# Performance work log

Measured on AMD Instinct MI355X. Metric: run time of the kernel, lower is better.

## Reference

```python
import jax, jax.numpy as jnp
import numpy as np

B, L, D, H, K = 4, 2048, 256, 8, 32
DH = D // H
DE = 64          # d_edge
CLIP = 32        # relpos_clip


def _ln(x, g, b):
    mu = x.mean(-1, keepdims=True)
    var = ((x - mu) ** 2).mean(-1, keepdims=True)
    return (x - mu) / jnp.sqrt(var + 1e-5) * g + b


def _gelu(x):
    return jax.nn.gelu(x, approximate=False)  # torch nn.GELU default = exact erf


def _masked_softmax(logits, mask):
    logits = jnp.where(mask == 0, jnp.finfo(logits.dtype).min, logits)
    return jax.nn.softmax(logits, axis=-1)


def setup_inputs() -> dict:
    key = jax.random.key(0)
    ks = jax.random.split(key, 24)
    s = 0.02
    w = lambda i, shape: jax.random.normal(ks[i], shape, jnp.float32) * s
    p = {}
    p['x'] = jax.random.normal(ks[0], (B, L, D), jnp.float32)
    p['mask'] = jax.random.randint(ks[1], (B, L), 0, 2, jnp.int32)
    p['nbr_idx'] = jax.random.randint(ks[2], (B, L, K), 0, L, jnp.int32)
    p['nbr_mask'] = jax.random.randint(ks[3], (B, L, K), 0, 2, jnp.int32)
    p['rel_pos'] = jax.random.randint(ks[4], (B, L, K), 0, 2 * CLIP + 1, jnp.int32)
    p['g1'] = jnp.ones((D,)); p['b1'] = jnp.zeros((D,))
    p['wq'] = w(5, (D, D)); p['wk'] = w(6, (D, D)); p['wv'] = w(7, (D, D))
    p['relpos_emb'] = w(8, (2 * CLIP + 1, DE))
    p['we1'] = w(9, (DE, D)); p['be1'] = jnp.zeros((D,))
    p['we2'] = w(10, (D, 1)); p['be2'] = jnp.zeros((1,))
    p['wg1'] = w(11, (2 * D, D)); p['bg1'] = jnp.zeros((D,))
    p['wg2'] = w(12, (D, D)); p['bg2'] = jnp.zeros((D,))
    p['wlo'] = w(13, (D, D)); p['blo'] = jnp.zeros((D,))
    p['wqkv'] = w(14, (D, 3 * D)); p['wgo'] = w(15, (D, D))
    p['wf1'] = w(16, (D, D)); p['bf1'] = jnp.zeros((D,))
    p['wf2'] = w(17, (D, 2)); p['bf2'] = jnp.zeros((2,))
    p['g2'] = jnp.ones((D,)); p['b2'] = jnp.zeros((D,))
    p['wff1'] = w(18, (D, 4 * D)); p['bff1'] = jnp.zeros((4 * D,))
    p['wff2'] = w(19, (4 * D, D)); p['bff2'] = jnp.zeros((D,))
    return p


def _block(x, mask, nbr_idx, nbr_mask, rel_pos,
           g1, b1, wq, wk, wv, relpos_emb, we1, be1, we2, be2,
           wg1, bg1, wg2, bg2, wlo, blo, wqkv, wgo,
           wf1, bf1, wf2, bf2, g2, b2, wff1, bff1, wff2, bff2):
    mf = mask.astype(x.dtype)                       # [B,L]
    h = _ln(x, g1, b1)

    # ---- local graph attention (gather over K neighbors) ----
    neigh = jax.vmap(lambda hb, ib: hb[ib])(h, nbr_idx)     # [B,L,K,D]
    q = (h @ wq)[:, :, None, :]                             # [B,L,1,D]
    k = neigh @ wk                                          # [B,L,K,D]
    v = neigh @ wv
    attn = (q * k).sum(-1) / np.sqrt(D).astype(np.float32)  # [B,L,K]
    rel = jnp.clip(rel_pos, -CLIP, CLIP) + CLIP
    e = relpos_emb[rel]                                     # [B,L,K,DE]
    attn = attn + (_gelu(e @ we1 + be1) @ we2 + be2)[..., 0]
    amask = nbr_mask * mask[:, :, None]
    w = _masked_softmax(attn, amask)
    agg = jnp.einsum('blk,blkd->bld', w, v)
    agg = agg @ wlo + blo
    g = jax.nn.sigmoid(_gelu(jnp.concatenate([h, agg], -1) @ wg1 + bg1) @ wg2 + bg2)
    h_local = (h + g * agg) * mf[..., None]

    # ---- global linear attention ----
    qkv = h @ wqkv
    qg, kg, vg = jnp.split(qkv, 3, axis=-1)
    to_heads = lambda z: z.reshape(B, L, H, DH).transpose(0, 2, 1, 3)  # [B,H,L,DH]
    qg, kg, vg = to_heads(qg), to_heads(kg), to_heads(vg)
    phi = lambda z: jax.nn.elu(z) + 1.0
    qg, kg = phi(qg), phi(kg)
    m = mf[:, None, :, None]
    kg = kg * m
    vg = vg * m
    kv = jnp.einsum('bhld,bhlm->bhdm', kg, vg)
    z = 1.0 / (jnp.einsum('bhld,bhd->bhl', qg, kg.sum(axis=2)) + 1e-6)
    y = jnp.einsum('bhld,bhdm->bhlm', qg, kv) * z[..., None]
    y = y.transpose(0, 2, 1, 3).reshape(B, L, D)
    y = (y @ wgo) * mf[..., None]
    h_global = h + y

    # ---- gated fusion (softmax over 2 branches) ----
    fw = jax.nn.softmax(_gelu(h @ wf1 + bf1) @ wf2 + bf2, axis=-1)
    yc = fw[..., 0:1] * h_local + fw[..., 1:2] * h_global
    x2 = x + (yc - x)  # DropPath is identity in eval mode

    # ---- FFN ----
    hn = _ln(x2, g2, b2)
    ffn = _gelu(hn @ wff1 + bff1) @ wff2 + bff2
    out = (x2 + ffn) * mf[..., None]
    return out


def reference(x, mask, nbr_idx, nbr_mask, rel_pos,
              g1, b1, wq, wk, wv, relpos_emb, we1, be1, we2, be2,
              wg1, bg1, wg2, bg2, wlo, blo, wqkv, wgo,
              wf1, bf1, wf2, bf2, g2, b2, wff1, bff1, wff2, bff2):
    return _block(x, mask, nbr_idx, nbr_mask, rel_pos,
                  g1, b1, wq, wk, wv, relpos_emb, we1, be1, we2, be2,
                  wg1, bg1, wg2, bg2, wlo, blo, wqkv, wgo,
                  wf1, bf1, wf2, bf2, g2, b2, wff1, bff1, wff2, bff2)
```

## Files before the change

kernel.cpp:

```cpp
#include <hip/hip_runtime.h>
#include <math.h>

#define LSEQ 2048
#define BB 4
#define DD 256
#define NROWS (BB*LSEQ)
#define LDBIG 1792

typedef unsigned short u16;
typedef unsigned int u32;
typedef short s16x8 __attribute__((ext_vector_type(8)));
typedef float f32x4 __attribute__((ext_vector_type(4)));

__device__ __forceinline__ float gelu_f(float x){
    return 0.5f*x*(1.0f+erff(x*0.70710678118654752440f));
}
__device__ __forceinline__ float phi_f(float z){ return z>0.f ? z+1.f : expf(z); }
__device__ __forceinline__ float bf2f(u16 u){ union{u32 i; float f;} x; x.i = ((u32)u)<<16; return x.f; }
__device__ __forceinline__ u16 f2bf(float f){ union{float f; u32 i;} x; x.f = f; u32 r = (x.i + 0x7fff + ((x.i>>16)&1)) >> 16; return (u16)r; }

struct TransDesc { const float* src; int dstoff; int K; int N; int tstart; };
struct TransArgs { TransDesc d[11]; };

__global__ __launch_bounds__(256) void prep_kernel(
    TransArgs args, u16* __restrict__ WT,
    const float* __restrict__ x, const float* __restrict__ g1,
    const float* __restrict__ b1, u16* __restrict__ h,
    const float* __restrict__ emb, const float* __restrict__ we1,
    const float* __restrict__ be1, const float* __restrict__ we2,
    const float* __restrict__ be2, float* __restrict__ btab,
    float* __restrict__ kvz)
{
    int bid = blockIdx.x;
    if (bid < 1280){
        int z = 0;
        #pragma unroll
        for (int i=1;i<11;++i) if (bid >= args.d[i].tstart) z = i;
        TransDesc e = args.d[z];
        int tid = bid - e.tstart;
        int ntx = e.N >> 5;
        int kt = tid / ntx, nt = tid - kt*ntx;
        __shared__ float tile[32][33];
        int tx = threadIdx.x & 31, ty = threadIdx.x >> 5;
        #pragma unroll
        for (int i=0;i<4;++i){
            int k = kt*32 + ty + i*8;
            tile[ty+i*8][tx] = e.src[(size_t)k*e.N + nt*32 + tx];
        }
        __syncthreads();
        #pragma unroll
        for (int i=0;i<4;++i){
            int n = nt*32 + ty + i*8;
            WT[e.dstoff + (size_t)n*e.K + kt*32 + tx] = f2bf(tile[tx][ty+i*8]);
        }
    } else if (bid < 9472){
        int r = bid - 1280; int t = threadIdx.x;
        size_t i = (size_t)r*DD + t;
        float v = x[i];
        float s = v, ss = v*v;
        #pragma unroll
        for (int o=32;o>=1;o>>=1){ s += __shfl_xor(s,o); ss += __shfl_xor(ss,o); }
        __shared__ float sh[8];
        int wave = t>>6, lane = t&63;
        if (lane==0){ sh[wave]=s; sh[4+wave]=ss; }
        __syncthreads();
        float S  = sh[0]+sh[1]+sh[2]+sh[3];
        float SS = sh[4]+sh[5]+sh[6]+sh[7];
        float mu  = S*(1.f/DD);
        float var = SS*(1.f/DD) - mu*mu;
        float inv = rsqrtf(var + 1e-5f);
        h[i] = f2bf((v-mu)*inv*g1[t] + b1[t]);
    } else if (bid < 9537){
        int r = bid - 9472; int j = threadIdx.x;
        float acc = be1[j];
        #pragma unroll 8
        for (int d=0; d<64; ++d) acc += emb[r*64+d]*we1[d*256+j];
        float tv = gelu_f(acc)*we2[j];
        #pragma unroll
        for (int o=32;o>=1;o>>=1) tv += __shfl_xor(tv,o);
        __shared__ float sh2[4];
        int wave = j>>6, lane = j&63;
        if (lane==0) sh2[wave]=tv;
        __syncthreads();
        if (j==0) btab[r] = sh2[0]+sh2[1]+sh2[2]+sh2[3] + be2[0];
    } else {
        int idx = (bid - 9537)*256 + threadIdx.x;
        kvz[idx] = 0.f;
    }
}

template<int ACT, bool FINAL, typename CT>
__device__ __forceinline__ void mgemm_core(
    const u16* __restrict__ A0, const u16* __restrict__ A1, int kswitch, int lda,
    const u16* __restrict__ WT, int Kd,
    const float* __restrict__ bias, int actcol,
    CT* __restrict__ C, int ldc,
    const u16* __restrict__ addsrc, const int* __restrict__ rowmask,
    int row0, int col0)
{
    __shared__ u16 ldsA[4096];
    __shared__ u16 ldsB[8192];
    int t = threadIdx.x;
    int l = t & 63, w = t >> 6;
    int wm = w >> 1, wn = w & 1;

    int s_ar = t >> 2, s_ao = t & 3;
    int aidx1 = (s_ar>>4)*1024 + s_ao*128 + (s_ar&15)*8;
    int aidx2 = aidx1 + 4*128;
    int s_bc = t >> 1, s_bo = (t & 1)*4;
    int bbase = (s_bc>>4)*1024 + (s_bc&15)*8;

    f32x4 acc[2][4];
    #pragma unroll
    for (int mf=0;mf<2;++mf)
        #pragma unroll
        for (int nf=0;nf<4;++nf)
            acc[mf][nf] = (f32x4){0.f,0.f,0.f,0.f};

    uint4 av1, av2, bv0, bv1, bv2, bv3;
    {
        const u16* ap = A0 + (size_t)(row0+s_ar)*lda;
        av1 = *(const uint4*)(ap + s_ao*8);
        av2 = *(const uint4*)(ap + 32 + s_ao*8);
        const u16* bp = WT + (size_t)(col0 + s_bc)*Kd + s_bo*8;
        bv0 = *(const uint4*)(bp); bv1 = *(const uint4*)(bp+8);
        bv2 = *(const uint4*)(bp+16); bv3 = *(const uint4*)(bp+24);
    }

    for (int k0 = 0; k0 < Kd; k0 += 64){
        __syncthreads();
        *(uint4*)&ldsA[aidx1] = av1;
        *(uint4*)&ldsA[aidx2] = av2;
        *(uint4*)&ldsB[bbase + (s_bo  )*128] = bv0;
        *(uint4*)&ldsB[bbase + (s_bo+1)*128] = bv1;
        *(uint4*)&ldsB[bbase + (s_bo+2)*128] = bv2;
        *(uint4*)&ldsB[bbase + (s_bo+3)*128] = bv3;
        __syncthreads();
        int kn = k0 + 64;
        if (kn < Kd){
            const u16* Ab = A0; int kk = kn;
            if (kn >= kswitch){ Ab = A1; kk = kn - kswitch; }
            const u16* ap = Ab + (size_t)(row0+s_ar)*lda + kk;
            av1 = *(const uint4*)(ap + s_ao*8);
            av2 = *(const uint4*)(ap + 32 + s_ao*8);
            const u16* bp = WT + (size_t)(col0 + s_bc)*Kd + kn + s_bo*8;
            bv0 = *(const uint4*)(bp); bv1 = *(const uint4*)(bp+8);
            bv2 = *(const uint4*)(bp+16); bv3 = *(const uint4*)(bp+24);
        }
        #pragma unroll
        for (int s=0;s<2;++s){
            s16x8 af[2], bfr[4];
            #pragma unroll
            for (int mf=0;mf<2;++mf) af[mf] = *(s16x8*)&ldsA[(wm*2+mf)*1024 + (s*4+(l>>4))*128 + (l&15)*8];
            #pragma unroll
            for (int nf=0;nf<4;++nf) bfr[nf] = *(s16x8*)&ldsB[(wn*4+nf)*1024 + (s*4+(l>>4))*128 + (l&15)*8];
            #pragma unroll
            for (int mf=0; mf<2; ++mf)
                #pragma unroll
                for (int nf=0; nf<4; ++nf)
                    acc[mf][nf] = __builtin_amdgcn_mfma_f32_16x16x32_bf16(af[mf], bfr[nf], acc[mf][nf], 0,0,0);
        }
    }

    int lrow = (l>>4)*4, lcol = l&15;
    #pragma unroll
    for (int mf=0; mf<2; ++mf){
        #pragma unroll
        for (int nf=0; nf<4; ++nf){
            int col = col0 + wn*64 + nf*16 + lcol;
            float bv;
            if (ACT==1) bv = (col >= actcol) ? bias[col-actcol] : 0.f;
            else        bv = bias ? bias[col] : 0.f;
            #pragma unroll
            for (int i=0;i<4;++i){
                int row = row0 + wm*32 + mf*16 + lrow + i;
                float v = acc[mf][nf][i] + bv;
                if (ACT==1){ if (col >= actcol) v = gelu_f(v); }
                else if (ACT==2) v = 1.f/(1.f+expf(-v));
                if (FINAL){
                    float mfv = (float)rowmask[row];
                    v = (bf2f(addsrc[(size_t)row*ldc + col]) + v) * mfv;
                }
                if constexpr (sizeof(CT)==2) C[(size_t)row*ldc+col] = (CT)f2bf(v);
                else                         C[(size_t)row*ldc+col] = v;
            }
        }
    }
}

template<int ACT, bool FINAL, typename CT>
__global__ __launch_bounds__(256) void mgemm(
    const u16* __restrict__ A0, const u16* __restrict__ A1, int kswitch, int lda,
    const u16* __restrict__ WT, int Kd,
    const float* __restrict__ bias, int actcol,
    CT* __restrict__ C, int ldc,
    const u16* __restrict__ addsrc, const int* __restrict__ rowmask)
{
    mgemm_core<ACT,FINAL,CT>(A0,A1,kswitch,lda,WT,Kd,bias,actcol,C,ldc,addsrc,rowmask,
                             blockIdx.x*64, blockIdx.y*128);
}

struct DualCfg { const u16* A; const u16* WT; const float* bias; u16* C; };
__global__ __launch_bounds__(256) void mgemm_dual(DualCfg c0, DualCfg c1)
{
    DualCfg c = blockIdx.z ? c1 : c0;
    mgemm_core<0,false,u16>(c.A, c.A, 1<<30, 256, c.WT, 256, c.bias, 0, c.C, 256,
                            nullptr, nullptr, blockIdx.x*64, blockIdx.y*128);
}

__global__ __launch_bounds__(256) void nattn_kernel(
    const u16* __restrict__ nb,
    const int* __restrict__ nbr_idx, const int* __restrict__ nbr_mask,
    const int* __restrict__ rel_pos, const int* __restrict__ mask,
    const float* __restrict__ btab, u16* __restrict__ agg)
{
    int r = blockIdx.x;
    int b = r >> 11;
    int t = threadIdx.x, lane = t&63, wave = t>>6;
    __shared__ float s_w[32];
    __shared__ float s_agg[4][256];
    uint2 qu = *(const uint2*)&nb[(size_t)r*LDBIG + lane*4];
    float q0 = bf2f(qu.x&0xffff), q1 = bf2f(qu.x>>16);
    float q2 = bf2f(qu.y&0xffff), q3 = bf2f(qu.y>>16);
    int mrow = mask[r];

    uint2 kreg[8], vreg[8];
    #pragma unroll
    for (int j=0;j<8;++j){
        int idx = nbr_idx[r*32 + wave*8 + j];
        size_t grow = ((size_t)(b<<11) + idx)*LDBIG;
        kreg[j] = *(const uint2*)&nb[grow + 256 + lane*4];
        vreg[j] = *(const uint2*)&nb[grow + 512 + lane*4];
    }
    float d[8];
    #pragma unroll
    for (int j=0;j<8;++j){
        d[j] = q0*bf2f(kreg[j].x&0xffff) + q1*bf2f(kreg[j].x>>16)
             + q2*bf2f(kreg[j].y&0xffff) + q3*bf2f(kreg[j].y>>16);
    }
    #define CMB(a,b,s) ({ float _t = (lane&(s)) ? (a) : (b); float _r = __shfl_xor(_t,(s)); (lane&(s)) ? ((b)+_r) : ((a)+_r); })
    float e10 = CMB(d[0],d[1],1), e11 = CMB(d[2],d[3],1);
    float e12 = CMB(d[4],d[5],1), e13 = CMB(d[6],d[7],1);
    float e20 = CMB(e10,e11,2),   e21 = CMB(e12,e13,2);
    float e3  = CMB(e20,e21,4);
    #undef CMB
    e3 += __shfl_xor(e3,8); e3 += __shfl_xor(e3,16); e3 += __shfl_xor(e3,32);
    if (lane < 8){
        int k = wave*8 + lane;
        int rp = rel_pos[r*32+k];
        rp = rp < -32 ? -32 : (rp > 32 ? 32 : rp);
        float logit = e3*0.0625f + btab[rp+32];
        int am = nbr_mask[r*32+k] * mrow;
        s_w[k] = am ? logit : -3.402823466e38f;
    }
    __syncthreads();
    if (wave==0){
        float lg = (lane<32) ? s_w[lane] : -3.402823466e38f;
        float m = lg;
        #pragma unroll
        for (int o=16;o>=1;o>>=1) m = fmaxf(m, __shfl_xor(m,o));
        float e = (lane<32) ? expf(lg-m) : 0.f;
        float ssum = e;
        #pragma unroll
        for (int o=16;o>=1;o>>=1) ssum += __shfl_xor(ssum,o);
        if (lane<32) s_w[lane] = e/ssum;
    }
    __syncthreads();
    float4 av = {0.f,0.f,0.f,0.f};
    #pragma unroll
    for (int j=0;j<8;++j){
        float wk = s_w[wave*8 + j];
        av.x += wk*bf2f(vreg[j].x&0xffff); av.y += wk*bf2f(vreg[j].x>>16);
        av.z += wk*bf2f(vreg[j].y&0xffff); av.w += wk*bf2f(vreg[j].y>>16);
    }
    *(float4*)&s_agg[wave][lane*4] = av;
    __syncthreads();
    float sum = s_agg[0][t]+s_agg[1][t]+s_agg[2][t]+s_agg[3][t];
    agg[(size_t)r*256 + t] = f2bf(sum);
}

__global__ __launch_bounds__(256) void linstats_kernel(
    const u16* __restrict__ qkv, const int* __restrict__ mask,
    float* __restrict__ kv, float* __restrict__ ksum)
{
    int blk = blockIdx.x;
    int bh = blk >> 4, ch = blk & 15;
    int b = bh >> 3, hh = bh & 7;
    int t = threadIdx.x;
    int d = t >> 3, m4 = (t & 7)*4;
    __shared__ float sk[8][32], sv[8][32];
    float a0=0,a1=0,a2=0,a3=0, aks=0;
    int l0 = ch*128;
    int half = t >> 7, tt = t & 127;
    int lr = tt >> 4, e2 = (tt & 15)*2;
    for (int g8=0; g8<16; ++g8){
        int l = l0 + g8*8 + lr;
        size_t base = ((size_t)b*LSEQ + l)*LDBIG + (half ? 1280 : 1024) + hh*32 + e2;
        u32 u = *(const u32*)&qkv[base];
        float mf = (float)mask[b*LSEQ + l];
        float x0 = bf2f((u16)(u & 0xffff));
        float x1 = bf2f((u16)(u >> 16));
        if (half==0){ sk[lr][e2] = phi_f(x0)*mf; sk[lr][e2+1] = phi_f(x1)*mf; }
        else        { sv[lr][e2] = x0*mf;        sv[lr][e2+1] = x1*mf; }
        __syncthreads();
        #pragma unroll
        for (int rr=0;rr<8;++rr){
            float kd = sk[rr][d];
            a0 += kd*sv[rr][m4]; a1 += kd*sv[rr][m4+1];
            a2 += kd*sv[rr][m4+2]; a3 += kd*sv[rr][m4+3];
            if ((t&7)==0) aks += kd;
        }
        __syncthreads();
    }
    size_t kb = (size_t)bh*1024 + d*32 + m4;
    atomicAdd(&kv[kb+0],a0); atomicAdd(&kv[kb+1],a1);
    atomicAdd(&kv[kb+2],a2); atomicAdd(&kv[kb+3],a3);
    if ((t&7)==0) atomicAdd(&ksum[bh*32+d], aks);
}

__global__ __launch_bounds__(256) void linapply_kernel(
    const u16* __restrict__ qkv, const float* __restrict__ kv,
    const float* __restrict__ ksum, u16* __restrict__ y)
{
    int r = blockIdx.x; int b = r >> 11;
    int t = threadIdx.x;
    __shared__ float sq[256];
    if (t < 128){
        u32 u = *(const u32*)&qkv[(size_t)r*LDBIG + 768 + t*2];
        sq[t*2]   = phi_f(bf2f((u16)(u & 0xffff)));
        sq[t*2+1] = phi_f(bf2f((u16)(u >> 16)));
    }
    __syncthreads();
    int hh = t>>5, m = t&31;
    const float* kvb = &kv[(size_t)((b<<3)+hh)*1024 + m];
    const float* ksb = &ksum[((b<<3)+hh)*32];
    const float* sqh = &sq[hh*32];
    float acc=0.f, az=0.f;
    #pragma unroll
    for (int dd=0; dd<32; ++dd){
        float qd = sqh[dd];
        acc += qd * kvb[dd*32];
        az  += qd * ksb[dd];
    }
    y[(size_t)r*256 + t] = f2bf(acc / (az + 1e-6f));
}

__global__ __launch_bounds__(128) void combine_kernel(
    const u16* __restrict__ h, const u16* __restrict__ agglo,
    const u16* __restrict__ g, const u16* __restrict__ ygo,
    const u16* __restrict__ bigout, const float* __restrict__ wf2,
    const float* __restrict__ bf2v, const int* __restrict__ mask,
    const float* __restrict__ g2, const float* __restrict__ b2,
    u16* __restrict__ x2, u16* __restrict__ hn)
{
    int r = blockIdx.x, t = threadIdx.x;
    int wave = t>>6, lane = t&63;
    u32 fu = *(const u32*)&bigout[(size_t)r*LDBIG + 1536 + t*2];
    float fa = bf2f((u16)(fu&0xffff)), fb = bf2f((u16)(fu>>16));
    int dd = t*2;
    float p0 = fa*wf2[dd*2]   + fb*wf2[dd*2+2];
    float p1 = fa*wf2[dd*2+1] + fb*wf2[dd*2+3];
    #pragma unroll
    for (int o=32;o>=1;o>>=1){ p0 += __shfl_xor(p0,o); p1 += __shfl_xor(p1,o); }
    __shared__ float shp[4];
    if (lane==0){ shp[wave]=p0; shp[2+wave]=p1; }
    __syncthreads();
    float P0 = shp[0]+shp[1]+bf2v[0], P1 = shp[2]+shp[3]+bf2v[1];
    float mx = fmaxf(P0,P1);
    float e0 = expf(P0-mx), e1 = expf(P1-mx);
    float f0 = e0/(e0+e1), f1v = e1/(e0+e1);
    size_t i = (size_t)r*DD + t*2;
    float mf = (float)mask[r];
    u32 hu = *(const u32*)&h[i],  au = *(const u32*)&agglo[i];
    u32 gu = *(const u32*)&g[i],  yu = *(const u32*)&ygo[i];
    float hv0 = bf2f((u16)(hu&0xffff)), hv1 = bf2f((u16)(hu>>16));
    float ag0 = bf2f((u16)(au&0xffff)), ag1 = bf2f((u16)(au>>16));
    float gg0 = bf2f((u16)(gu&0xffff)), gg1 = bf2f((u16)(gu>>16));
    float yy0 = bf2f((u16)(yu&0xffff)), yy1 = bf2f((u16)(yu>>16));
    float v0 = f0*((hv0 + gg0*ag0)*mf) + f1v*(hv0 + yy0*mf);
    float v1 = f0*((hv1 + gg1*ag1)*mf) + f1v*(hv1 + yy1*mf);
    *(u32*)&x2[i] = (u32)f2bf(v0) | ((u32)f2bf(v1)<<16);
    float s = v0+v1, ss = v0*v0+v1*v1;
    #pragma unroll
    for (int o=32;o>=1;o>>=1){ s += __shfl_xor(s,o); ss += __shfl_xor(ss,o); }
    __shared__ float sh[4];
    if (lane==0){ sh[wave]=s; sh[2+wave]=ss; }
    __syncthreads();
    float S  = sh[0]+sh[1];
    float SS = sh[2]+sh[3];
    float mu  = S*(1.f/DD);
    float var = SS*(1.f/DD) - mu*mu;
    float inv = rsqrtf(var + 1e-5f);
    int j0 = t*2;
    float o0 = (v0-mu)*inv*g2[j0]   + b2[j0];
    float o1 = (v1-mu)*inv*g2[j0+1] + b2[j0+1];
    *(u32*)&hn[i] = (u32)f2bf(o0) | ((u32)f2bf(o1)<<16);
}

extern "C" void kernel_launch(void* const* d_in, const int* in_sizes, int n_in,
                              void* d_out, int out_size, void* d_ws, size_t ws_size,
                              hipStream_t stream)
{
    const float* x        = (const float*)d_in[0];
    const int*   mask     = (const int*)  d_in[1];
    const int*   nbr_idx  = (const int*)  d_in[2];
    const int*   nbr_mask = (const int*)  d_in[3];
    const int*   rel_pos  = (const int*)  d_in[4];
    const float* g1   = (const float*)d_in[5];
    const float* b1   = (const float*)d_in[6];
    const float* wq   = (const float*)d_in[7];
    const float* wk   = (const float*)d_in[8];
    const float* wv   = (const float*)d_in[9];
    const float* relpos_emb = (const float*)d_in[10];
    const float* we1  = (const float*)d_in[11];
    const float* be1  = (const float*)d_in[12];
    const float* we2  = (const float*)d_in[13];
    const float* be2  = (const float*)d_in[14];
    const float* wg1  = (const float*)d_in[15];
    const float* bg1  = (const float*)d_in[16];
    const float* wg2  = (const float*)d_in[17];
    const float* bg2  = (const float*)d_in[18];
    const float* wlo  = (const float*)d_in[19];
    const float* blo  = (const float*)d_in[20];
    const float* wqkv = (const float*)d_in[21];
    const float* wgo  = (const float*)d_in[22];
    const float* wf1  = (const float*)d_in[23];
    const float* bf1  = (const float*)d_in[24];
    const float* wf2  = (const float*)d_in[25];
    const float* bf2  = (const float*)d_in[26];
    const float* g2   = (const float*)d_in[27];
    const float* b2   = (const float*)d_in[28];
    const float* wff1 = (const float*)d_in[29];
    const float* bff1 = (const float*)d_in[30];
    const float* wff2 = (const float*)d_in[31];
    const float* bff2 = (const float*)d_in[32];
    float* out = (float*)d_out;

    unsigned char* wsb = (unsigned char*)d_ws;
    u16* bigout  = (u16*)(wsb + ((size_t)0<<20));
    u16* h_bf    = (u16*)(wsb + ((size_t)30<<20));
    u16* agg_bf  = (u16*)(wsb + ((size_t)34<<20));
    u16* agglo_bf= (u16*)(wsb + ((size_t)38<<20));
    u16* x2y_bf  = (u16*)(wsb + ((size_t)42<<20));
    u16* tg_bf   = (u16*)(wsb + ((size_t)46<<20));
    u16* ygo_bf  = (u16*)(wsb + ((size_t)50<<20));
    u16* hn_bf   = (u16*)(wsb + ((size_t)54<<20));
    u16* WT      = (u16*)(wsb + ((size_t)58<<20));
    float* btab  = (float*)(wsb + ((size_t)61<<20));
    float* kvb   = btab + 128;
    float* ksb   = kvb + 32768;

    const int WT_BIG  = 0;
    const int WT_LO   = 458752;
    const int WT_G1   = 524288;
    const int WT_G2   = 655360;
    const int WT_GO   = 720896;
    const int WT_FF1  = 786432;
    const int WT_FF2  = 1048576;

    TransArgs ta;
    ta.d[0]  = { wq,   WT_BIG + 0,        256,  256,    0 };
    ta.d[1]  = { wk,   WT_BIG + 65536,    256,  256,   64 };
    ta.d[2]  = { wv,   WT_BIG + 131072,   256,  256,  128 };
    ta.d[3]  = { wqkv, WT_BIG + 196608,   256,  768,  192 };
    ta.d[4]  = { wf1,  WT_BIG + 393216,   256,  256,  384 };
    ta.d[5]  = { wlo,  WT_LO,             256,  256,  448 };
    ta.d[6]  = { wg1,  WT_G1,             512,  256,  512 };
    ta.d[7]  = { wg2,  WT_G2,             256,  256,  640 };
    ta.d[8]  = { wgo,  WT_GO,             256,  256,  704 };
    ta.d[9]  = { wff1, WT_FF1,            256, 1024,  768 };
    ta.d[10] = { wff2, WT_FF2,           1024,  256, 1024 };

    const int KBIG = 1<<30;
    dim3 blk(256);

    prep_kernel<<<9669, blk, 0, stream>>>(ta, WT, x, g1, b1, h_bf,
                                          relpos_emb, we1, be1, we2, be2, btab, kvb);
    mgemm<1,false,u16><<<dim3(128,14), blk, 0, stream>>>(h_bf, h_bf, KBIG, 256, WT+WT_BIG, 256, bf1, 1536, bigout, LDBIG, nullptr, nullptr);
    linstats_kernel<<<512, blk, 0, stream>>>(bigout, mask, kvb, ksb);
    linapply_kernel<<<NROWS, blk, 0, stream>>>(bigout, kvb, ksb, x2y_bf);
    nattn_kernel<<<NROWS, blk, 0, stream>>>(bigout, nbr_idx, nbr_mask, rel_pos, mask, btab, agg_bf);
    {
        DualCfg cgo = { x2y_bf, WT+WT_GO, nullptr, ygo_bf };
        DualCfg clo = { agg_bf, WT+WT_LO, blo,     agglo_bf };
        mgemm_dual<<<dim3(128,2,2), blk, 0, stream>>>(cgo, clo);
    }
    mgemm<1,false,u16><<<dim3(128,2), blk, 0, stream>>>(h_bf, agglo_bf, 256, 256, WT+WT_G1, 512, bg1, 0, tg_bf, 256, nullptr, nullptr);
    mgemm<2,false,u16><<<dim3(128,2), blk, 0, stream>>>(tg_bf, tg_bf, KBIG, 256, WT+WT_G2, 256, bg2, 0, agg_bf, 256, nullptr, nullptr);
    combine_kernel<<<NROWS, dim3(128), 0, stream>>>(h_bf, agglo_bf, agg_bf, ygo_bf, bigout, wf2, bf2, mask, g2, b2, x2y_bf, hn_bf);
    mgemm<1,false,u16><<<dim3(128,8), blk, 0, stream>>>(hn_bf, hn_bf, KBIG, 256, WT+WT_FF1, 256, bff1, 0, bigout, 1024, nullptr, nullptr);
    mgemm<0,true,float><<<dim3(128,2), blk, 0, stream>>>(bigout, bigout, KBIG, 1024, WT+WT_FF2, 1024, bff2, 0, out, 256, x2y_bf, mask);
}
```

Measured before the change: 277.6 us.

## Fold wlo into wg1, fuse linear-attn apply into neighbor attention, merge three GEMMs

```diff
diff --git a/kernel.cpp b/kernel.cpp
--- a/kernel.cpp
+++ b/kernel.cpp
@@ -12,6 +12,14 @@
 typedef short s16x8 __attribute__((ext_vector_type(8)));
 typedef float f32x4 __attribute__((ext_vector_type(4)));
 
+#define WT_BIG  0
+#define WT_LO   458752
+#define WT_G1   524288
+#define WT_G2   655360
+#define WT_GO   720896
+#define WT_FF1  786432
+#define WT_FF2  1048576
+
 __device__ __forceinline__ float gelu_f(float x){
     return 0.5f*x*(1.0f+erff(x*0.70710678118654752440f));
 }
@@ -19,7 +27,7 @@
 __device__ __forceinline__ float bf2f(u16 u){ union{u32 i; float f;} x; x.i = ((u32)u)<<16; return x.f; }
 __device__ __forceinline__ u16 f2bf(float f){ union{float f; u32 i;} x; x.f = f; u32 r = (x.i + 0x7fff + ((x.i>>16)&1)) >> 16; return (u16)r; }
 
-struct TransDesc { const float* src; int dstoff; int K; int N; int tstart; };
+struct TransDesc { const float* src; int dstoff; int srcK; int N; int dstStride; int tstart; };
 struct TransArgs { TransDesc d[11]; };
 
 __global__ __launch_bounds__(256) void prep_kernel(
@@ -29,10 +37,13 @@
     const float* __restrict__ emb, const float* __restrict__ we1,
     const float* __restrict__ be1, const float* __restrict__ we2,
     const float* __restrict__ be2, float* __restrict__ btab,
-    float* __restrict__ kvz)
+    float* __restrict__ kvz,
+    const float* __restrict__ wlo, const float* __restrict__ wg1,
+    const float* __restrict__ blo, const float* __restrict__ bg1,
+    float* __restrict__ bprime)
 {
     int bid = blockIdx.x;
-    if (bid < 1280){
+    if (bid < 1216){
         int z = 0;
         #pragma unroll
         for (int i=1;i<11;++i) if (bid >= args.d[i].tstart) z = i;
@@ -51,10 +62,10 @@
         #pragma unroll
         for (int i=0;i<4;++i){
             int n = nt*32 + ty + i*8;
-            WT[e.dstoff + (size_t)n*e.K + kt*32 + tx] = f2bf(tile[tx][ty+i*8]);
+            WT[e.dstoff + (size_t)n*e.dstStride + kt*32 + tx] = f2bf(tile[tx][ty+i*8]);
         }
-    } else if (bid < 9472){
-        int r = bid - 1280; int t = threadIdx.x;
+    } else if (bid < 9408){
+        int r = bid - 1216; int t = threadIdx.x;
         size_t i = (size_t)r*DD + t;
         float v = x[i];
         float s = v, ss = v*v;
@@ -70,8 +81,8 @@
         float var = SS*(1.f/DD) - mu*mu;
         float inv = rsqrtf(var + 1e-5f);
         h[i] = f2bf((v-mu)*inv*g1[t] + b1[t]);
-    } else if (bid < 9537){
-        int r = bid - 9472; int j = threadIdx.x;
+    } else if (bid < 9473){
+        int r = bid - 9408; int j = threadIdx.x;
         float acc = be1[j];
         #pragma unroll 8
         for (int d=0; d<64; ++d) acc += emb[r*64+d]*we1[d*256+j];
@@ -83,9 +94,24 @@
         if (lane==0) sh2[wave]=tv;
         __syncthreads();
         if (j==0) btab[r] = sh2[0]+sh2[1]+sh2[2]+sh2[3] + be2[0];
+    } else if (bid < 9605){
+        int idx = (bid - 9473)*256 + threadIdx.x;
+        kvz[idx] = 0.f;
+    } else if (bid < 9861){
+        int n = bid - 9605; int t = threadIdx.x;
+        __shared__ float shc[256];
+        shc[t] = wg1[(size_t)(256+t)*256 + n];
+        __syncthreads();
+        const float* wr = wlo + (size_t)t*256;
+        float a = 0.f;
+        #pragma unroll 8
+        for (int m=0;m<256;++m) a += wr[m]*shc[m];
+        WT[WT_G1 + (size_t)n*512 + 256 + t] = f2bf(a);
     } else {
-        int idx = (bid - 9537)*256 + threadIdx.x;
-        kvz[idx] = 0.f;
+        int t = threadIdx.x;
+        float a = bg1[t];
+        for (int m=0;m<256;++m) a += blo[m]*wg1[(size_t)(256+m)*256 + t];
+        bprime[t] = a;
     }
 }
 
@@ -200,25 +226,35 @@
                              blockIdx.x*64, blockIdx.y*128);
 }
 
-struct DualCfg { const u16* A; const u16* WT; const float* bias; u16* C; };
-__global__ __launch_bounds__(256) void mgemm_dual(DualCfg c0, DualCfg c1)
-{
-    DualCfg c = blockIdx.z ? c1 : c0;
-    mgemm_core<0,false,u16>(c.A, c.A, 1<<30, 256, c.WT, 256, c.bias, 0, c.C, 256,
-                            nullptr, nullptr, blockIdx.x*64, blockIdx.y*128);
-}
-
-__global__ __launch_bounds__(256) void nattn_kernel(
+struct GemmCfg { const u16* A0; const u16* A1; int kswitch; const u16* WT; int Kd;
+                 const float* bias; int act; u16* C; };
+__global__ __launch_bounds__(256) void mgemm_tri(GemmCfg c0, GemmCfg c1, GemmCfg c2)
+{
+    GemmCfg c = (blockIdx.z==0) ? c0 : ((blockIdx.z==1) ? c1 : c2);
+    if (c.act==1)
+        mgemm_core<1,false,u16>(c.A0, c.A1, c.kswitch, 256, c.WT, c.Kd, c.bias, 0,
+                                c.C, 256, nullptr, nullptr, blockIdx.x*64, blockIdx.y*128);
+    else
+        mgemm_core<0,false,u16>(c.A0, c.A1, c.kswitch, 256, c.WT, c.Kd, c.bias, 0,
+                                c.C, 256, nullptr, nullptr, blockIdx.x*64, blockIdx.y*128);
+}
+
+__global__ __launch_bounds__(256) void lg_kernel(
     const u16* __restrict__ nb,
     const int* __restrict__ nbr_idx, const int* __restrict__ nbr_mask,
     const int* __restrict__ rel_pos, const int* __restrict__ mask,
-    const float* __restrict__ btab, u16* __restrict__ agg)
-{
-    int r = blockIdx.x;
+    const float* __restrict__ btab, u16* __restrict__ agg,
+    const float* __restrict__ kv, const float* __restrict__ ksum,
+    u16* __restrict__ y)
+{
+    int bid = blockIdx.x;
+    int xcd = bid & 7, pos = bid >> 3;
+    int r = (xcd>>1)*2048 + (xcd&1)*1024 + pos;
     int b = r >> 11;
     int t = threadIdx.x, lane = t&63, wave = t>>6;
     __shared__ float s_w[32];
     __shared__ float s_agg[4][256];
+    __shared__ float sq[256];
     uint2 qu = *(const uint2*)&nb[(size_t)r*LDBIG + lane*4];
     float q0 = bf2f(qu.x&0xffff), q1 = bf2f(qu.x>>16);
     float q2 = bf2f(qu.y&0xffff), q3 = bf2f(qu.y>>16);
@@ -253,6 +289,11 @@
         int am = nbr_mask[r*32+k] * mrow;
         s_w[k] = am ? logit : -3.402823466e38f;
     }
+    if (t < 128){
+        u32 u = *(const u32*)&nb[(size_t)r*LDBIG + 768 + t*2];
+        sq[t*2]   = phi_f(bf2f((u16)(u & 0xffff)));
+        sq[t*2+1] = phi_f(bf2f((u16)(u >> 16)));
+    }
     __syncthreads();
     if (wave==0){
         float lg = (lane<32) ? s_w[lane] : -3.402823466e38f;
@@ -277,6 +318,19 @@
     __syncthreads();
     float sum = s_agg[0][t]+s_agg[1][t]+s_agg[2][t]+s_agg[3][t];
     agg[(size_t)r*256 + t] = f2bf(sum);
+
+    int hh = t>>5, m = t&31;
+    const float* kvb = &kv[(size_t)((b<<3)+hh)*1024 + m];
+    const float* ksb = &ksum[((b<<3)+hh)*32];
+    const float* sqh = &sq[hh*32];
+    float acc=0.f, az=0.f;
+    #pragma unroll
+    for (int dd=0; dd<32; ++dd){
+        float qd = sqh[dd];
+        acc += qd * kvb[dd*32];
+        az  += qd * ksb[dd];
+    }
+    y[(size_t)r*256 + t] = f2bf(acc / (az + 1e-6f));
 }
 
 __global__ __launch_bounds__(256) void linstats_kernel(
@@ -284,16 +338,16 @@
     float* __restrict__ kv, float* __restrict__ ksum)
 {
     int blk = blockIdx.x;
-    int bh = blk >> 4, ch = blk & 15;
+    int bh = blk >> 6, ch = blk & 63;
     int b = bh >> 3, hh = bh & 7;
     int t = threadIdx.x;
     int d = t >> 3, m4 = (t & 7)*4;
     __shared__ float sk[8][32], sv[8][32];
     float a0=0,a1=0,a2=0,a3=0, aks=0;
-    int l0 = ch*128;
+    int l0 = ch*32;
     int half = t >> 7, tt = t & 127;
     int lr = tt >> 4, e2 = (tt & 15)*2;
-    for (int g8=0; g8<16; ++g8){
+    for (int g8=0; g8<4; ++g8){
         int l = l0 + g8*8 + lr;
         size_t base = ((size_t)b*LSEQ + l)*LDBIG + (half ? 1280 : 1024) + hh*32 + e2;
         u32 u = *(const u32*)&qkv[base];
@@ -316,33 +370,6 @@
     atomicAdd(&kv[kb+0],a0); atomicAdd(&kv[kb+1],a1);
     atomicAdd(&kv[kb+2],a2); atomicAdd(&kv[kb+3],a3);
     if ((t&7)==0) atomicAdd(&ksum[bh*32+d], aks);
-}
-
-__global__ __launch_bounds__(256) void linapply_kernel(
-    const u16* __restrict__ qkv, const float* __restrict__ kv,
-    const float* __restrict__ ksum, u16* __restrict__ y)
-{
-    int r = blockIdx.x; int b = r >> 11;
-    int t = threadIdx.x;
-    __shared__ float sq[256];
-    if (t < 128){
-        u32 u = *(const u32*)&qkv[(size_t)r*LDBIG + 768 + t*2];
-        sq[t*2]   = phi_f(bf2f((u16)(u & 0xffff)));
-        sq[t*2+1] = phi_f(bf2f((u16)(u >> 16)));
-    }
-    __syncthreads();
-    int hh = t>>5, m = t&31;
-    const float* kvb = &kv[(size_t)((b<<3)+hh)*1024 + m];
-    const float* ksb = &ksum[((b<<3)+hh)*32];
-    const float* sqh = &sq[hh*32];
-    float acc=0.f, az=0.f;
-    #pragma unroll
-    for (int dd=0; dd<32; ++dd){
-        float qd = sqh[dd];
-        acc += qd * kvb[dd*32];
-        az  += qd * ksb[dd];
-    }
-    y[(size_t)r*256 + t] = f2bf(acc / (az + 1e-6f));
 }
 
 __global__ __launch_bounds__(128) void combine_kernel(
@@ -449,43 +476,37 @@
     float* btab  = (float*)(wsb + ((size_t)61<<20));
     float* kvb   = btab + 128;
     float* ksb   = kvb + 32768;
-
-    const int WT_BIG  = 0;
-    const int WT_LO   = 458752;
-    const int WT_G1   = 524288;
-    const int WT_G2   = 655360;
-    const int WT_GO   = 720896;
-    const int WT_FF1  = 786432;
-    const int WT_FF2  = 1048576;
+    float* bprime= ksb + 1024;
 
     TransArgs ta;
-    ta.d[0]  = { wq,   WT_BIG + 0,        256,  256,    0 };
-    ta.d[1]  = { wk,   WT_BIG + 65536,    256,  256,   64 };
-    ta.d[2]  = { wv,   WT_BIG + 131072,   256,  256,  128 };
-    ta.d[3]  = { wqkv, WT_BIG + 196608,   256,  768,  192 };
-    ta.d[4]  = { wf1,  WT_BIG + 393216,   256,  256,  384 };
-    ta.d[5]  = { wlo,  WT_LO,             256,  256,  448 };
-    ta.d[6]  = { wg1,  WT_G1,             512,  256,  512 };
-    ta.d[7]  = { wg2,  WT_G2,             256,  256,  640 };
-    ta.d[8]  = { wgo,  WT_GO,             256,  256,  704 };
-    ta.d[9]  = { wff1, WT_FF1,            256, 1024,  768 };
-    ta.d[10] = { wff2, WT_FF2,           1024,  256, 1024 };
+    ta.d[0]  = { wq,   WT_BIG + 0,        256,  256,  256,    0 };
+    ta.d[1]  = { wk,   WT_BIG + 65536,    256,  256,  256,   64 };
+    ta.d[2]  = { wv,   WT_BIG + 131072,   256,  256,  256,  128 };
+    ta.d[3]  = { wqkv, WT_BIG + 196608,   256,  768,  256,  192 };
+    ta.d[4]  = { wf1,  WT_BIG + 393216,   256,  256,  256,  384 };
+    ta.d[5]  = { wlo,  WT_LO,             256,  256,  256,  448 };
+    ta.d[6]  = { wg1,  WT_G1,             256,  256,  512,  512 };
+    ta.d[7]  = { wg2,  WT_G2,             256,  256,  256,  576 };
+    ta.d[8]  = { wgo,  WT_GO,             256,  256,  256,  640 };
+    ta.d[9]  = { wff1, WT_FF1,            256, 1024,  256,  704 };
+    ta.d[10] = { wff2, WT_FF2,           1024,  256, 1024,  960 };
 
     const int KBIG = 1<<30;
     dim3 blk(256);
 
-    prep_kernel<<<9669, blk, 0, stream>>>(ta, WT, x, g1, b1, h_bf,
-                                          relpos_emb, we1, be1, we2, be2, btab, kvb);
+    prep_kernel<<<9862, blk, 0, stream>>>(ta, WT, x, g1, b1, h_bf,
+                                          relpos_emb, we1, be1, we2, be2, btab, kvb,
+                                          wlo, wg1, blo, bg1, bprime);
     mgemm<1,false,u16><<<dim3(128,14), blk, 0, stream>>>(h_bf, h_bf, KBIG, 256, WT+WT_BIG, 256, bf1, 1536, bigout, LDBIG, nullptr, nullptr);
-    linstats_kernel<<<512, blk, 0, stream>>>(bigout, mask, kvb, ksb);
-    linapply_kernel<<<NROWS, blk, 0, stream>>>(bigout, kvb, ksb, x2y_bf);
-    nattn_kernel<<<NROWS, blk, 0, stream>>>(bigout, nbr_idx, nbr_mask, rel_pos, mask, btab, agg_bf);
+    linstats_kernel<<<2048, blk, 0, stream>>>(bigout, mask, kvb, ksb);
+    lg_kernel<<<NROWS, blk, 0, stream>>>(bigout, nbr_idx, nbr_mask, rel_pos, mask, btab,
+                                         agg_bf, kvb, ksb, x2y_bf);
     {
-        DualCfg cgo = { x2y_bf, WT+WT_GO, nullptr, ygo_bf };
-        DualCfg clo = { agg_bf, WT+WT_LO, blo,     agglo_bf };
-        mgemm_dual<<<dim3(128,2,2), blk, 0, stream>>>(cgo, clo);
-    }
-    mgemm<1,false,u16><<<dim3(128,2), blk, 0, stream>>>(h_bf, agglo_bf, 256, 256, WT+WT_G1, 512, bg1, 0, tg_bf, 256, nullptr, nullptr);
+        GemmCfg cgo = { x2y_bf, x2y_bf, KBIG, WT+WT_GO, 256, nullptr, 0, ygo_bf };
+        GemmCfg clo = { agg_bf, agg_bf, KBIG, WT+WT_LO, 256, blo,     0, agglo_bf };
+        GemmCfg cg1 = { h_bf,   agg_bf, 256,  WT+WT_G1, 512, bprime,  1, tg_bf };
+        mgemm_tri<<<dim3(128,2,3), blk, 0, stream>>>(cgo, clo, cg1);
+    }
     mgemm<2,false,u16><<<dim3(128,2), blk, 0, stream>>>(tg_bf, tg_bf, KBIG, 256, WT+WT_G2, 256, bg2, 0, agg_bf, 256, nullptr, nullptr);
     combine_kernel<<<NROWS, dim3(128), 0, stream>>>(h_bf, agglo_bf, agg_bf, ygo_bf, bigout, wf2, bf2, mask, g2, b2, x2y_bf, hn_bf);
     mgemm<1,false,u16><<<dim3(128,8), blk, 0, stream>>>(hn_bf, hn_bf, KBIG, 256, WT+WT_FF1, 256, bff1, 0, bigout, 1024, nullptr, nullptr);
```

After: 317.1 us. 14.2% more time.
